# Kernel tuning notes

Hardware: AMD Instinct MI355X
Metric: run time of the kernel (lower is better)

## Reference

```python
import jax, jax.numpy as jnp
import numpy as np

B, C, H, W = 16, 512, 64, 64   # C == e_dim
N_E = 256                       # codebook size
BETA = 0.25


def setup_inputs() -> dict:
    key = jax.random.key(0)
    k1, k2, k3 = jax.random.split(key, 3)
    z = jax.random.normal(k1, (B, C, H, W), dtype=jnp.float32)
    # nn.Embedding init: uniform(-1/n_e, 1/n_e)
    emb_weight = jax.random.uniform(k2, (N_E, C), dtype=jnp.float32,
                                    minval=-1.0 / N_E, maxval=1.0 / N_E)
    std_param = jnp.array(1.0, dtype=jnp.float32)
    means = jnp.zeros((3,), dtype=jnp.float32)
    conv_w = jax.random.normal(k3, (C, C), dtype=jnp.float32) * 0.02  # 1x1 conv kernel [out,in]
    conv_b = jnp.zeros((C,), dtype=jnp.float32)
    return {"z": z, "emb_weight": emb_weight, "std_param": std_param,
            "means": means, "conv_w": conv_w, "conv_b": conv_b}


def reference(z, emb_weight, std_param, means, conv_w, conv_b):
    # torch uses .item() on std/mean -> detached scalars
    std = jax.lax.stop_gradient(jnp.abs(std_param))
    mean = jax.lax.stop_gradient(jnp.mean(means))
    w = emb_weight * std + mean                      # [n_e, C] scaled codebook

    zf = z.transpose(0, 2, 3, 1).reshape(-1, C)       # [N, C], N = B*H*W
    # pairwise squared L2: ||z||^2 + ||w||^2 - 2 z.w
    d = (jnp.sum(zf * zf, axis=1, keepdims=True)
         + jnp.sum(w * w, axis=1)
         - 2.0 * zf @ w.T)                            # [N, n_e]
    idx = jnp.argmin(d, axis=1)                       # [N]
    one_hot = jax.nn.one_hot(idx, N_E, dtype=z.dtype) # [N, n_e]

    z_q = (one_hot @ w).reshape(B, H, W, C).transpose(0, 3, 1, 2)  # [B,C,H,W]

    sg = jax.lax.stop_gradient
    loss = jnp.mean((sg(z_q) - z) ** 2) + BETA * jnp.mean((z_q - sg(z)) ** 2)

    z_q = z + sg(z_q - z)                             # straight-through

    e_mean = jnp.mean(one_hot, axis=0)                # [n_e]
    perplexity = jnp.exp(-jnp.sum(e_mean * jnp.log(e_mean + 1e-10)))

    # 1x1 conv == channel matmul
    out = jnp.einsum('bchw,oc->bohw', z_q, conv_w) + conv_b[None, :, None, None]
    return out, loss, perplexity
```

## Files before the change

### kernel.cpp

```cpp
#include <hip/hip_runtime.h>


#define C_DIM 512
#define N_E   256
#define HW    4096
#define SAr   72

typedef unsigned short u16;
typedef u16   u16x4 __attribute__((ext_vector_type(4)));
typedef u16   u16x8 __attribute__((ext_vector_type(8)));
typedef short s16x8 __attribute__((ext_vector_type(8)));
typedef float f32x4 __attribute__((ext_vector_type(4)));

__device__ __forceinline__ u16 f2bf(float f) {
    unsigned u = __float_as_uint(f);
    return (u16)((u + 0x7FFFu + ((u >> 16) & 1u)) >> 16);
}

__global__ void prep_w(const float* __restrict__ emb, const float* __restrict__ stdp,
                       const float* __restrict__ means,
                       u16* __restrict__ wfrag, float* __restrict__ wnorm,
                       float* __restrict__ accum, unsigned int* __restrict__ hist) {
    int c = blockIdx.x;
    int t = threadIdx.x;
    if (c == 0) {
        hist[t] = 0u;
        if (t < 2) accum[t] = 0.f;
    }
    float stdv = fabsf(stdp[0]);
    float meanv = (means[0] + means[1] + means[2]) * (1.0f / 3.0f);
    float ss = 0.f;
    for (int k = t; k < C_DIM; k += 256) {
        float w = emb[c * C_DIM + k] * stdv + meanv;
        ss += w * w;
        int ntg  = c >> 4;
        int lane = (c & 15) | (((k >> 3) & 3) << 4);
        int ksg  = k >> 5;
        int j    = k & 7;
        wfrag[((ntg * 16 + ksg) * 64 + lane) * 8 + j] = f2bf(w);
    }
    #pragma unroll
    for (int m = 1; m < 64; m <<= 1) ss += __shfl_xor(ss, m, 64);
    __shared__ float red[4];
    if ((t & 63) == 0) red[t >> 6] = ss;
    __syncthreads();
    if (t == 0) wnorm[c] = red[0] + red[1] + red[2] + red[3];
}

__global__ __launch_bounds__(64)
void prep_m(const float* __restrict__ convw, const u16* __restrict__ wfrag,
            const float* __restrict__ convb, float* __restrict__ M2T) {
    int lane = threadIdx.x;
    int m15 = lane & 15, quad = lane >> 4;
    int o0 = blockIdx.x * 32;
    const u16x8* wf8 = (const u16x8*)wfrag;

    f32x4 acc[2][16];
    #pragma unroll
    for (int mt = 0; mt < 2; ++mt)
        #pragma unroll
        for (int nt = 0; nt < 16; ++nt)
            acc[mt][nt] = (f32x4){0.f, 0.f, 0.f, 0.f};

    for (int ksg = 0; ksg < 16; ++ksg) {
        s16x8 am[2];
        #pragma unroll
        for (int mt = 0; mt < 2; ++mt) {
            const float* p = convw + (o0 + mt * 16 + m15) * C_DIM + ksg * 32 + quad * 8;
            f32x4 a = *(const f32x4*)p, b = *(const f32x4*)(p + 4);
            union { u16x8 v8; u16 s[8]; } ua;
            #pragma unroll
            for (int j = 0; j < 4; ++j) { ua.s[j] = f2bf(a[j]); ua.s[4 + j] = f2bf(b[j]); }
            am[mt] = __builtin_bit_cast(s16x8, ua.v8);
        }
        #pragma unroll
        for (int nt = 0; nt < 16; ++nt) {
            s16x8 bfr = __builtin_bit_cast(s16x8, wf8[(nt * 16 + ksg) * 64 + lane]);
            #pragma unroll
            for (int mt = 0; mt < 2; ++mt)
                acc[mt][nt] = __builtin_amdgcn_mfma_f32_16x16x32_bf16(am[mt], bfr, acc[mt][nt], 0, 0, 0);
        }
    }
    #pragma unroll
    for (int mt = 0; mt < 2; ++mt)
        #pragma unroll
        for (int r = 0; r < 4; ++r) {
            int o = o0 + mt * 16 + quad * 4 + r;
            float cb = convb[o];
            #pragma unroll
            for (int nt = 0; nt < 16; ++nt)
                M2T[o * N_E + nt * 16 + m15] = acc[mt][nt][r] + cb;
        }
}

__global__ __launch_bounds__(256, 2)
void argmin_k(const float* __restrict__ z, const u16* __restrict__ wfrag,
              const float* __restrict__ wnorm, u16* __restrict__ idxs,
              float* __restrict__ accum, unsigned int* __restrict__ hist) {
    __shared__ u16 Ab[2][128 * SAr];
    __shared__ unsigned long long lmin[128];
    __shared__ unsigned int lhist[N_E];
    __shared__ float lred[8];

    int tid = threadIdx.x;
    int wave = tid >> 6, lane = tid & 63;
    int mhalf = wave & 1, nhalf = wave >> 1;
    int bb = blockIdx.x;
    const float* zb = z + (size_t)(bb >> 5) * (C_DIM * HW) + (bb & 31) * 128;

    if (tid < 128) lmin[tid] = ~0ull;
    lhist[tid] = 0u;

    f32x4 acc[4][8];
    #pragma unroll
    for (int mt = 0; mt < 4; ++mt)
        #pragma unroll
        for (int nt = 0; nt < 8; ++nt)
            acc[mt][nt] = (f32x4){0.f, 0.f, 0.f, 0.f};

    int t5 = tid & 31, cg = tid >> 5;
    const float* gsrc = zb + (size_t)(cg * 8) * HW + t5 * 4;
    int skey = (t5 >> 1) & 7;
    int wch  = (cg * 8) ^ (skey * 8);
    float zs = 0.f;

    int m15 = lane & 15, quad = lane >> 4;
    const u16x8* wf8 = (const u16x8*)wfrag;

    f32x4 sv[8];
    #pragma unroll
    for (int i = 0; i < 8; ++i) sv[i] = *(const f32x4*)(gsrc + (size_t)i * HW);
    #pragma unroll
    for (int p = 0; p < 4; ++p) {
        u16x8 pk;
        #pragma unroll
        for (int i = 0; i < 8; ++i) { float f = sv[i][p]; zs += f * f; pk[i] = f2bf(f); }
        *(u16x8*)(&Ab[0][(t5 * 4 + p) * SAr + wch]) = pk;
    }

    for (int kc = 0; kc < 8; ++kc) {
        int cur = kc & 1;
        if (kc < 7) {
            const float* g2 = gsrc + (size_t)((kc + 1) * 64) * HW;
            #pragma unroll
            for (int i = 0; i < 8; ++i) sv[i] = *(const f32x4*)(g2 + (size_t)i * HW);
        }
        __syncthreads();
        #pragma unroll
        for (int ks = 0; ks < 2; ++ks) {
            s16x8 bfr[8];
            #pragma unroll
            for (int nt = 0; nt < 8; ++nt) {
                int ntg = nhalf * 8 + nt, ksg = kc * 2 + ks;
                bfr[nt] = __builtin_bit_cast(s16x8, wf8[(ntg * 16 + ksg) * 64 + lane]);
            }
            s16x8 am[4];
            #pragma unroll
            for (int mt = 0; mt < 4; ++mt) {
                int pos = mhalf * 64 + mt * 16 + m15;
                int rkey = (mt * 2 + (m15 >> 3)) & 7;
                int rch = (ks * 32 + quad * 8) ^ (rkey * 8);
                am[mt] = __builtin_bit_cast(s16x8, *(const u16x8*)(&Ab[cur][pos * SAr + rch]));
            }
            #pragma unroll
            for (int mt = 0; mt < 4; ++mt)
                #pragma unroll
                for (int nt = 0; nt < 8; ++nt)
                    acc[mt][nt] = __builtin_amdgcn_mfma_f32_16x16x32_bf16(
                        am[mt], bfr[nt], acc[mt][nt], 0, 0, 0);
        }
        if (kc < 7) {
            #pragma unroll
            for (int p = 0; p < 4; ++p) {
                u16x8 pk;
                #pragma unroll
                for (int i = 0; i < 8; ++i) { float f = sv[i][p]; zs += f * f; pk[i] = f2bf(f); }
                *(u16x8*)(&Ab[cur ^ 1][(t5 * 4 + p) * SAr + wch]) = pk;
            }
        }
    }

    float wn[8];
    #pragma unroll
    for (int nt = 0; nt < 8; ++nt) wn[nt] = wnorm[(nhalf * 8 + nt) * 16 + m15];

    #pragma unroll
    for (int mt = 0; mt < 4; ++mt) {
        #pragma unroll
        for (int r = 0; r < 4; ++r) {
            unsigned long long key = ~0ull;
            #pragma unroll
            for (int nt = 0; nt < 8; ++nt) {
                float d = wn[nt] - 2.0f * acc[mt][nt][r];
                unsigned u = __float_as_uint(d);
                u ^= (u >> 31) ? 0xFFFFFFFFu : 0x80000000u;
                unsigned code = (unsigned)((nhalf * 8 + nt) * 16 + m15);
                unsigned long long k2 = ((unsigned long long)u << 32) | code;
                key = (k2 < key) ? k2 : key;
            }
            #pragma unroll
            for (int sm = 1; sm < 16; sm <<= 1) {
                unsigned long long o2 = (unsigned long long)__shfl_xor((long long)key, sm, 64);
                key = (o2 < key) ? o2 : key;
            }
            if (m15 == 0) {
                int pos = mhalf * 64 + mt * 16 + quad * 4 + r;
                atomicMin(&lmin[pos], key);
            }
        }
    }
    __syncthreads();

    float dsum = 0.f;
    if (tid < 128) {
        unsigned long long key = lmin[tid];
        unsigned code = (unsigned)(key & 0xFFFFu);
        unsigned u = (unsigned)(key >> 32);
        u ^= (u >> 31) ? 0x80000000u : 0xFFFFFFFFu;
        dsum = __uint_as_float(u);
        idxs[bb * 128 + tid] = (u16)code;
        atomicAdd(&lhist[code], 1u);
    }
    #pragma unroll
    for (int sm = 1; sm < 64; sm <<= 1) {
        dsum += __shfl_xor(dsum, sm, 64);
        zs   += __shfl_xor(zs, sm, 64);
    }
    if (lane == 0) { lred[wave] = dsum; lred[4 + wave] = zs; }
    __syncthreads();
    if (tid == 0) {
        atomicAdd(&accum[0], lred[4] + lred[5] + lred[6] + lred[7]);
        atomicAdd(&accum[1], lred[0] + lred[1] + lred[2] + lred[3]);
    }
    unsigned cnt = lhist[tid];
    if (cnt) atomicAdd(&hist[tid], cnt);
}

__global__ __launch_bounds__(256)
void out_k(const float* __restrict__ M2T, const u16* __restrict__ idxs,
           float* __restrict__ out, const float* __restrict__ accum,
           const unsigned int* __restrict__ hist) {
    __shared__ float col[N_E];
    int tid = threadIdx.x;
    int bk = blockIdx.x;
    int o = bk & 511, b = bk >> 9;
    col[tid] = M2T[o * N_E + tid];
    __syncthreads();
    size_t obase = (size_t)b * (C_DIM * HW) + (size_t)o * HW;
    #pragma unroll
    for (int j = 0; j < 4; ++j) {
        int p4 = (j * 256 + tid) * 4;
        u16x4 ids = *(const u16x4*)(idxs + b * HW + p4);
        f32x4 r;
        #pragma unroll
        for (int jj = 0; jj < 4; ++jj) r[jj] = col[ids[jj]];
        *(f32x4*)(out + obase + p4) = r;
    }
    if (bk == 0) {
        float e = (float)hist[tid] * (1.0f / 65536.0f);
        float term = e * logf(e + 1e-10f);
        #pragma unroll
        for (int m = 1; m < 64; m <<= 1) term += __shfl_xor(term, m, 64);
        __shared__ float red[4];
        if ((tid & 63) == 0) red[tid >> 6] = term;
        __syncthreads();
        if (tid == 0) {
            float s = red[0] + red[1] + red[2] + red[3];
            out[33554432] = 1.25f * (accum[0] + accum[1]) * (1.0f / 33554432.0f);
            out[33554433] = expf(-s);
        }
    }
}

extern "C" void kernel_launch(void* const* d_in, const int* in_sizes, int n_in,
                              void* d_out, int out_size, void* d_ws, size_t ws_size,
                              hipStream_t stream) {
    (void)in_sizes; (void)n_in; (void)out_size; (void)ws_size;
    const float* z     = (const float*)d_in[0];
    const float* emb   = (const float*)d_in[1];
    const float* stdp  = (const float*)d_in[2];
    const float* means = (const float*)d_in[3];
    const float* convw = (const float*)d_in[4];
    const float* convb = (const float*)d_in[5];

    char* ws = (char*)d_ws;
    u16*   wfrag = (u16*)(ws + 0);
    float* wnorm = (float*)(ws + 262144);
    float* M2T   = (float*)(ws + 263168);
    u16*   idxs  = (u16*)(ws + 787456);
    float* accum = (float*)(ws + 918528);
    unsigned int* hist = (unsigned int*)(ws + 918536);
    float* out = (float*)d_out;

    prep_w  <<<256,  256, 0, stream>>>(emb, stdp, means, wfrag, wnorm, accum, hist);
    prep_m  <<<16,    64, 0, stream>>>(convw, wfrag, convb, M2T);
    argmin_k<<<512,  256, 0, stream>>>(z, wfrag, wnorm, idxs, accum, hist);
    out_k   <<<8192, 256, 0, stream>>>(M2T, idxs, out, accum, hist);
}
```

Before: 289.4 us.

## Fuse codebook-conv output gather into argmin kernel and merge prep kernels

Merges the two prep kernels into one launch, with the conv-weight times codebook product now computed in fp32 FMA by extra blocks instead of a separate bf16 MFMA kernel. The output gather is moved into the argmin kernel: each block keeps its 128 codes in shared memory and writes all 512 output channels directly, removing the idxs round trip and the 8192-block out kernel. A tiny final kernel computes loss and perplexity. The fused epilogue adds a long store phase to each argmin block, gathering M2T from global/L2, and its occupancy is limited to two blocks per CU, which may reduce store overlap.

```diff
diff --git a/kernel.cpp b/kernel.cpp
--- a/kernel.cpp
+++ b/kernel.cpp
@@ -17,90 +17,76 @@
     return (u16)((u + 0x7FFFu + ((u >> 16) & 1u)) >> 16);
 }
 
-__global__ void prep_w(const float* __restrict__ emb, const float* __restrict__ stdp,
-                       const float* __restrict__ means,
-                       u16* __restrict__ wfrag, float* __restrict__ wnorm,
-                       float* __restrict__ accum, unsigned int* __restrict__ hist) {
-    int c = blockIdx.x;
+__global__ __launch_bounds__(256)
+void prep(const float* __restrict__ emb, const float* __restrict__ stdp,
+          const float* __restrict__ means, const float* __restrict__ convw,
+          const float* __restrict__ convb,
+          u16* __restrict__ wfrag, float* __restrict__ wnorm,
+          float* __restrict__ M2T, float* __restrict__ accum,
+          unsigned int* __restrict__ hist) {
     int t = threadIdx.x;
-    if (c == 0) {
-        hist[t] = 0u;
-        if (t < 2) accum[t] = 0.f;
-    }
-    float stdv = fabsf(stdp[0]);
+    float stdv  = fabsf(stdp[0]);
     float meanv = (means[0] + means[1] + means[2]) * (1.0f / 3.0f);
-    float ss = 0.f;
-    for (int k = t; k < C_DIM; k += 256) {
-        float w = emb[c * C_DIM + k] * stdv + meanv;
-        ss += w * w;
-        int ntg  = c >> 4;
-        int lane = (c & 15) | (((k >> 3) & 3) << 4);
-        int ksg  = k >> 5;
-        int j    = k & 7;
-        wfrag[((ntg * 16 + ksg) * 64 + lane) * 8 + j] = f2bf(w);
-    }
-    #pragma unroll
-    for (int m = 1; m < 64; m <<= 1) ss += __shfl_xor(ss, m, 64);
-    __shared__ float red[4];
-    if ((t & 63) == 0) red[t >> 6] = ss;
-    __syncthreads();
-    if (t == 0) wnorm[c] = red[0] + red[1] + red[2] + red[3];
-}
-
-__global__ __launch_bounds__(64)
-void prep_m(const float* __restrict__ convw, const u16* __restrict__ wfrag,
-            const float* __restrict__ convb, float* __restrict__ M2T) {
-    int lane = threadIdx.x;
-    int m15 = lane & 15, quad = lane >> 4;
-    int o0 = blockIdx.x * 32;
-    const u16x8* wf8 = (const u16x8*)wfrag;
-
-    f32x4 acc[2][16];
-    #pragma unroll
-    for (int mt = 0; mt < 2; ++mt)
-        #pragma unroll
-        for (int nt = 0; nt < 16; ++nt)
-            acc[mt][nt] = (f32x4){0.f, 0.f, 0.f, 0.f};
-
-    for (int ksg = 0; ksg < 16; ++ksg) {
-        s16x8 am[2];
-        #pragma unroll
-        for (int mt = 0; mt < 2; ++mt) {
-            const float* p = convw + (o0 + mt * 16 + m15) * C_DIM + ksg * 32 + quad * 8;
-            f32x4 a = *(const f32x4*)p, b = *(const f32x4*)(p + 4);
-            union { u16x8 v8; u16 s[8]; } ua;
-            #pragma unroll
-            for (int j = 0; j < 4; ++j) { ua.s[j] = f2bf(a[j]); ua.s[4 + j] = f2bf(b[j]); }
-            am[mt] = __builtin_bit_cast(s16x8, ua.v8);
-        }
-        #pragma unroll
-        for (int nt = 0; nt < 16; ++nt) {
-            s16x8 bfr = __builtin_bit_cast(s16x8, wf8[(nt * 16 + ksg) * 64 + lane]);
-            #pragma unroll
-            for (int mt = 0; mt < 2; ++mt)
-                acc[mt][nt] = __builtin_amdgcn_mfma_f32_16x16x32_bf16(am[mt], bfr, acc[mt][nt], 0, 0, 0);
-        }
-    }
-    #pragma unroll
-    for (int mt = 0; mt < 2; ++mt)
-        #pragma unroll
-        for (int r = 0; r < 4; ++r) {
-            int o = o0 + mt * 16 + quad * 4 + r;
-            float cb = convb[o];
-            #pragma unroll
-            for (int nt = 0; nt < 16; ++nt)
-                M2T[o * N_E + nt * 16 + m15] = acc[mt][nt][r] + cb;
-        }
+
+    if (blockIdx.x < 256) {
+        int c = blockIdx.x;
+        if (c == 0) {
+            hist[t] = 0u;
+            if (t < 2) accum[t] = 0.f;
+        }
+        float ss = 0.f;
+        for (int k = t; k < C_DIM; k += 256) {
+            float w = emb[c * C_DIM + k] * stdv + meanv;
+            ss += w * w;
+            int ntg  = c >> 4;
+            int lane = (c & 15) | (((k >> 3) & 3) << 4);
+            int ksg  = k >> 5;
+            int j    = k & 7;
+            wfrag[((ntg * 16 + ksg) * 64 + lane) * 8 + j] = f2bf(w);
+        }
+        #pragma unroll
+        for (int m = 1; m < 64; m <<= 1) ss += __shfl_xor(ss, m, 64);
+        __shared__ float red[4];
+        if ((t & 63) == 0) red[t >> 6] = ss;
+        __syncthreads();
+        if (t == 0) wnorm[c] = red[0] + red[1] + red[2] + red[3];
+    } else {
+        __shared__ float cw[4][C_DIM];
+        int o0 = (blockIdx.x - 256) * 4;
+        for (int i = t; i < 4 * C_DIM; i += 256)
+            cw[i >> 9][i & 511] = convw[(o0 + (i >> 9)) * C_DIM + (i & 511)];
+        __syncthreads();
+        float a0 = 0.f, a1 = 0.f, a2 = 0.f, a3 = 0.f;
+        const float* er = emb + t * C_DIM;
+        #pragma unroll 4
+        for (int k = 0; k < C_DIM; k += 4) {
+            f32x4 ev = *(const f32x4*)(er + k);
+            #pragma unroll
+            for (int jj = 0; jj < 4; ++jj) {
+                float w = ev[jj] * stdv + meanv;
+                a0 += cw[0][k + jj] * w;
+                a1 += cw[1][k + jj] * w;
+                a2 += cw[2][k + jj] * w;
+                a3 += cw[3][k + jj] * w;
+            }
+        }
+        M2T[(o0 + 0) * N_E + t] = a0 + convb[o0 + 0];
+        M2T[(o0 + 1) * N_E + t] = a1 + convb[o0 + 1];
+        M2T[(o0 + 2) * N_E + t] = a2 + convb[o0 + 2];
+        M2T[(o0 + 3) * N_E + t] = a3 + convb[o0 + 3];
+    }
 }
 
 __global__ __launch_bounds__(256, 2)
-void argmin_k(const float* __restrict__ z, const u16* __restrict__ wfrag,
-              const float* __restrict__ wnorm, u16* __restrict__ idxs,
-              float* __restrict__ accum, unsigned int* __restrict__ hist) {
+void argmin_out(const float* __restrict__ z, const u16* __restrict__ wfrag,
+                const float* __restrict__ wnorm, const float* __restrict__ M2T,
+                float* __restrict__ out,
+                float* __restrict__ accum, unsigned int* __restrict__ hist) {
     __shared__ u16 Ab[2][128 * SAr];
     __shared__ unsigned long long lmin[128];
     __shared__ unsigned int lhist[N_E];
     __shared__ float lred[8];
+    __shared__ u16 lcode[128];
 
     int tid = threadIdx.x;
     int wave = tid >> 6, lane = tid & 63;
@@ -218,7 +204,7 @@
         unsigned u = (unsigned)(key >> 32);
         u ^= (u >> 31) ? 0x80000000u : 0xFFFFFFFFu;
         dsum = __uint_as_float(u);
-        idxs[bb * 128 + tid] = (u16)code;
+        lcode[tid] = (u16)code;
         atomicAdd(&lhist[code], 1u);
     }
     #pragma unroll
@@ -234,41 +220,37 @@
     }
     unsigned cnt = lhist[tid];
     if (cnt) atomicAdd(&hist[tid], cnt);
+
+    int t5o = tid & 31, oo = tid >> 5;
+    int ec[4];
+    #pragma unroll
+    for (int jj = 0; jj < 4; ++jj) ec[jj] = (int)lcode[t5o * 4 + jj];
+    float* obase = out + ((size_t)(bb >> 5) * C_DIM + oo) * HW + (bb & 31) * 128 + t5o * 4;
+    const float* m2 = M2T + oo * N_E;
+    #pragma unroll 4
+    for (int og = 0; og < C_DIM; og += 8) {
+        f32x4 r;
+        #pragma unroll
+        for (int jj = 0; jj < 4; ++jj) r[jj] = m2[og * N_E + ec[jj]];
+        *(f32x4*)(obase + (size_t)og * HW) = r;
+    }
 }
 
 __global__ __launch_bounds__(256)
-void out_k(const float* __restrict__ M2T, const u16* __restrict__ idxs,
-           float* __restrict__ out, const float* __restrict__ accum,
-           const unsigned int* __restrict__ hist) {
-    __shared__ float col[N_E];
+void fin_k(const float* __restrict__ accum, const unsigned int* __restrict__ hist,
+           float* __restrict__ out) {
     int tid = threadIdx.x;
-    int bk = blockIdx.x;
-    int o = bk & 511, b = bk >> 9;
-    col[tid] = M2T[o * N_E + tid];
+    float e = (float)hist[tid] * (1.0f / 65536.0f);
+    float term = e * logf(e + 1e-10f);
+    #pragma unroll
+    for (int m = 1; m < 64; m <<= 1) term += __shfl_xor(term, m, 64);
+    __shared__ float red[4];
+    if ((tid & 63) == 0) red[tid >> 6] = term;
     __syncthreads();
-    size_t obase = (size_t)b * (C_DIM * HW) + (size_t)o * HW;
-    #pragma unroll
-    for (int j = 0; j < 4; ++j) {
-        int p4 = (j * 256 + tid) * 4;
-        u16x4 ids = *(const u16x4*)(idxs + b * HW + p4);
-        f32x4 r;
-        #pragma unroll
-        for (int jj = 0; jj < 4; ++jj) r[jj] = col[ids[jj]];
-        *(f32x4*)(out + obase + p4) = r;
-    }
-    if (bk == 0) {
-        float e = (float)hist[tid] * (1.0f / 65536.0f);
-        float term = e * logf(e + 1e-10f);
-        #pragma unroll
-        for (int m = 1; m < 64; m <<= 1) term += __shfl_xor(term, m, 64);
-        __shared__ float red[4];
-        if ((tid & 63) == 0) red[tid >> 6] = term;
-        __syncthreads();
-        if (tid == 0) {
-            float s = red[0] + red[1] + red[2] + red[3];
-            out[33554432] = 1.25f * (accum[0] + accum[1]) * (1.0f / 33554432.0f);
-            out[33554433] = expf(-s);
-        }
+    if (tid == 0) {
+        float s = red[0] + red[1] + red[2] + red[3];
+        out[33554432] = 1.25f * (accum[0] + accum[1]) * (1.0f / 33554432.0f);
+        out[33554433] = expf(-s);
     }
 }
 
@@ -287,13 +269,12 @@
     u16*   wfrag = (u16*)(ws + 0);
     float* wnorm = (float*)(ws + 262144);
     float* M2T   = (float*)(ws + 263168);
-    u16*   idxs  = (u16*)(ws + 787456);
-    float* accum = (float*)(ws + 918528);
-    unsigned int* hist = (unsigned int*)(ws + 918536);
+    float* accum = (float*)(ws + 787456);
+    unsigned int* hist = (unsigned int*)(ws + 787464);
     float* out = (float*)d_out;
 
-    prep_w  <<<256,  256, 0, stream>>>(emb, stdp, means, wfrag, wnorm, accum, hist);
-    prep_m  <<<16,    64, 0, stream>>>(convw, wfrag, convb, M2T);
-    argmin_k<<<512,  256, 0, stream>>>(z, wfrag, wnorm, idxs, accum, hist);
-    out_k   <<<8192, 256, 0, stream>>>(M2T, idxs, out, accum, hist);
-}
+    prep      <<<384, 256, 0, stream>>>(emb, stdp, means, convw, convb,
+                                        wfrag, wnorm, M2T, accum, hist);
+    argmin_out<<<512, 256, 0, stream>>>(z, wfrag, wnorm, M2T, out, accum, hist);
+    fin_k     <<<1,   256, 0, stream>>>(accum, hist, out);
+}
```

Result: slower. 301.8 us (+4.3%).
